# Kernel tuning notes

Measured on AMD Instinct MI355X. Metric: run time of the kernel, lower is better.

## Reference

```python
import jax, jax.numpy as jnp
import numpy as np

EMB_DIM = 256
N_EMBED = 1024
BETA = 0.25


def setup_inputs() -> dict:
    key = jax.random.key(0)
    k1, k2 = jax.random.split(key)
    encoderout = jax.random.normal(k1, (32, EMB_DIM, 32, 32), dtype=jnp.float32)
    # embedding.weight.data.normal_(mean=0, std=1/n_embed)
    codebook = jax.random.normal(k2, (N_EMBED, EMB_DIM), dtype=jnp.float32) * (1.0 / N_EMBED)
    return {"encoderout": encoderout, "codebook": codebook}


def reference(encoderout, codebook):
    # NCHW -> NHWC
    x = jnp.transpose(encoderout, (0, 2, 3, 1))  # [B,H,W,D]
    flat = x.reshape(-1, EMB_DIM)                # [N,D]
    d2 = (jnp.sum(flat * flat, axis=1, keepdims=True)
          + jnp.sum(codebook * codebook, axis=1)[None, :]
          - 2.0 * flat @ codebook.T)             # [N,K]
    idx = jnp.argmin(d2, axis=1)                 # [N]
    quant = codebook[idx].reshape(x.shape)       # [B,H,W,D]
    codebook_loss = jnp.mean((quant - jax.lax.stop_gradient(x)) ** 2)
    commitment_loss = jnp.mean((x - jax.lax.stop_gradient(quant)) ** 2)
    loss = codebook_loss + BETA * commitment_loss
    # FAITHFUL to source bug: straight-through output is overwritten by the
    # input permuted back to NCHW, so out == encoderout.
    out = jnp.transpose(x, (0, 3, 1, 2))
    return (out, loss, codebook_loss, commitment_loss)
```

## Files before the change

### kernel.cpp

```cpp
#include <hip/hip_runtime.h>
#include <stdint.h>


#define EMB 256
#define ELEMS 8388608
#define NBLK 256

typedef __bf16 bf16x8 __attribute__((ext_vector_type(8)));
typedef float  f32x4  __attribute__((ext_vector_type(4)));

union Frag { uint4 u4; bf16x8 v; };

__device__ __forceinline__ unsigned short f2bf(float f) {
    unsigned u = __float_as_uint(f);
    u += 0x7FFFu + ((u >> 16) & 1u);
    return (unsigned short)(u >> 16);
}

__global__ __launch_bounds__(256) void vq_prep(const float* __restrict__ cb,
                                               uint2* __restrict__ cbswz,
                                               float* __restrict__ esq,
                                               float* __restrict__ accum,
                                               unsigned* __restrict__ done) {
    if (blockIdx.x == 0 && threadIdx.x == 0) { accum[0] = 0.f; done[0] = 0u; }

    const int tid  = threadIdx.x;
    const int w    = tid >> 6;
    const int lane = tid & 63;
    const int n    = blockIdx.x * 4 + w;

    const float4* row = (const float4*)(cb + n * EMB);
    float4 v = row[lane];

    float s = v.x * v.x + v.y * v.y + v.z * v.z + v.w * v.w;
    #pragma unroll
    for (int m = 1; m <= 32; m <<= 1) s += __shfl_xor(s, m);
    if (lane == 0) esq[n] = s;

    unsigned lo = (unsigned)f2bf(v.x) | ((unsigned)f2bf(v.y) << 16);
    unsigned hi = (unsigned)f2bf(v.z) | ((unsigned)f2bf(v.w) << 16);
    const int kc = lane >> 1;
    const int h  = lane & 1;
    const unsigned idx4 = ((unsigned)(n >> 6) << 11) + ((unsigned)(kc >> 2) << 8)
                        + ((unsigned)(n & 63) << 2) + (unsigned)(kc & 3);
    cbswz[idx4 * 2 + h] = make_uint2(lo, hi);
}


#define CHUNK_BODY(nc_, LOADNEXT_) do {                                        \
    f32x4 _a0 = (f32x4){0.f,0.f,0.f,0.f};                                      \
    f32x4 _a1 = (f32x4){0.f,0.f,0.f,0.f};                                      \
    f32x4 _a2 = (f32x4){0.f,0.f,0.f,0.f};                                      \
    f32x4 _a3 = (f32x4){0.f,0.f,0.f,0.f};                                      \
    _Pragma("unroll")                                                          \
    for (int _ks = 0; _ks < 8; ++_ks) {                                        \
        bf16x8 _bv = bfr[_ks].v;                                               \
        _a0 = __builtin_amdgcn_mfma_f32_16x16x32_bf16(afr[0][_ks], _bv, _a0, 0, 0, 0); \
        _a1 = __builtin_amdgcn_mfma_f32_16x16x32_bf16(afr[1][_ks], _bv, _a1, 0, 0, 0); \
        _a2 = __builtin_amdgcn_mfma_f32_16x16x32_bf16(afr[2][_ks], _bv, _a2, 0, 0, 0); \
        _a3 = __builtin_amdgcn_mfma_f32_16x16x32_bf16(afr[3][_ks], _bv, _a3, 0, 0, 0); \
        if (LOADNEXT_)       \
            bfr[_ks].u4 = pc[((nc_) + 1) * 2048 + _ks * 256];                  \
    }                                                                          \
    const float _eq = esq[(nc_) * 64 + nl];                                    \
    _Pragma("unroll")                                                          \
    for (int _r2 = 0; _r2 < 4; ++_r2) {                                        \
        rmin[0][_r2] = fminf(rmin[0][_r2], fmaf(-2.f, _a0[_r2], _eq));         \
        rmin[1][_r2] = fminf(rmin[1][_r2], fmaf(-2.f, _a1[_r2], _eq));         \
        rmin[2][_r2] = fminf(rmin[2][_r2], fmaf(-2.f, _a2[_r2], _eq));         \
        rmin[3][_r2] = fminf(rmin[3][_r2], fmaf(-2.f, _a3[_r2], _eq));         \
    } } while (0)

__global__ __launch_bounds__(512, 2)
void vq_main(const float* __restrict__ enc,
             const uint4* __restrict__ cbswz,
             const float* __restrict__ esq,
             float* __restrict__ out,
             float* __restrict__ accum,
             unsigned* __restrict__ done) {
    __shared__ uint4 As[4096];
    __shared__ float dmin[4][128];
    __shared__ float partsA[8];
    __shared__ float partsB[2];

    const int tid  = threadIdx.x;
    const int w    = tid >> 6;
    const int lane = tid & 63;
    const int q    = lane >> 4;
    const int c    = lane & 15;
    const int wm   = w >> 2;
    const int wn   = w & 3;

    const int b   = blockIdx.x >> 3;
    const int hw0 = (blockIdx.x & 7) << 7;
    const float* encB = enc + (size_t)b * 262144 + hw0;
    float*       outB = out + (size_t)b * 262144 + hw0;

    const int nl = wn * 16 + c;
    const uint4* pc = cbswz + (size_t)(nl * 4 + q);

    const int q4 = tid & 31;
    const int kg = tid >> 5;
    float sx = 0.f;
    {
        f32x4 vh[16];
        #pragma unroll
        for (int j = 0; j < 16; ++j)
            vh[j] = *(const f32x4*)(encB + (size_t)(kg * 16 + j) * 1024 + q4 * 4);
        #pragma unroll
        for (int j = 0; j < 16; ++j) {
            *(f32x4*)(outB + (size_t)(kg * 16 + j) * 1024 + q4 * 4) = vh[j];
            #pragma unroll
            for (int i2 = 0; i2 < 4; ++i2) sx = fmaf(vh[j][i2], vh[j][i2], sx);
        }
        #pragma unroll
        for (int i = 0; i < 4; ++i) {
            unsigned short us[16];
            #pragma unroll
            for (int j = 0; j < 16; ++j) us[j] = f2bf(vh[j][i]);
            uint4 pk0, pk1;
            pk0.x = (unsigned)us[0]  | ((unsigned)us[1]  << 16);
            pk0.y = (unsigned)us[2]  | ((unsigned)us[3]  << 16);
            pk0.z = (unsigned)us[4]  | ((unsigned)us[5]  << 16);
            pk0.w = (unsigned)us[6]  | ((unsigned)us[7]  << 16);
            pk1.x = (unsigned)us[8]  | ((unsigned)us[9]  << 16);
            pk1.y = (unsigned)us[10] | ((unsigned)us[11] << 16);
            pk1.z = (unsigned)us[12] | ((unsigned)us[13] << 16);
            pk1.w = (unsigned)us[14] | ((unsigned)us[15] << 16);
            const int r = q4 * 4 + i;
            As[r * 32 + ((2 * kg + 0) ^ (r & 7))] = pk0;
            As[r * 32 + ((2 * kg + 1) ^ (r & 7))] = pk1;
        }
    }

    Frag bfr[8];
    #pragma unroll
    for (int ks = 0; ks < 8; ++ks) bfr[ks].u4 = pc[ks * 256];

    #pragma unroll
    for (int m = 1; m <= 32; m <<= 1) sx += __shfl_xor(sx, m);
    if (lane == 0) partsA[w] = sx;
    __syncthreads();

    bf16x8 afr[4][8];
    #pragma unroll
    for (int mi = 0; mi < 4; ++mi) {
        const int r = wm * 64 + mi * 16 + c;
        #pragma unroll
        for (int ks = 0; ks < 8; ++ks) {
            Frag fa; fa.u4 = As[r * 32 + ((ks * 4 + q) ^ (r & 7))];
            afr[mi][ks] = fa.v;
        }
    }

    float rmin[4][4];
    #pragma unroll
    for (int mi = 0; mi < 4; ++mi)
        #pragma unroll
        for (int r2 = 0; r2 < 4; ++r2) rmin[mi][r2] = 1e30f;

    for (int nc = 0; nc < 15; ++nc) CHUNK_BODY(nc, 1);
    CHUNK_BODY(15, 0);

    #pragma unroll
    for (int mi = 0; mi < 4; ++mi)
        #pragma unroll
        for (int r2 = 0; r2 < 4; ++r2) {
            float x = rmin[mi][r2];
            x = fminf(x, __shfl_xor(x, 1));
            x = fminf(x, __shfl_xor(x, 2));
            x = fminf(x, __shfl_xor(x, 4));
            x = fminf(x, __shfl_xor(x, 8));
            rmin[mi][r2] = x;
        }
    if (c == 0) {
        #pragma unroll
        for (int mi = 0; mi < 4; ++mi)
            #pragma unroll
            for (int r2 = 0; r2 < 4; ++r2)
                dmin[wn][wm * 64 + mi * 16 + q * 4 + r2] = rmin[mi][r2];
    }
    __syncthreads();

    if (tid < 128) {
        float vr = fminf(fminf(dmin[0][tid], dmin[1][tid]),
                         fminf(dmin[2][tid], dmin[3][tid]));
        #pragma unroll
        for (int m = 1; m <= 32; m <<= 1) vr += __shfl_xor(vr, m);
        if ((tid & 63) == 0) partsB[tid >> 6] = vr;
    }
    __syncthreads();

    if (tid == 0) {
        float s = partsB[0] + partsB[1];
        #pragma unroll
        for (int w2 = 0; w2 < 8; ++w2) s += partsA[w2];
        atomicAdd(accum, s);
        __threadfence();
        unsigned prev = atomicAdd(done, 1u);
        if (prev == NBLK - 1) {
            float tot = atomicAdd(accum, 0.0f);
            float cbl = tot * (1.0f / (float)ELEMS);
            out[ELEMS + 0] = 1.25f * cbl;
            out[ELEMS + 1] = cbl;
            out[ELEMS + 2] = cbl;
        }
    }
}

extern "C" void kernel_launch(void* const* d_in, const int* in_sizes, int n_in,
                              void* d_out, int out_size, void* d_ws, size_t ws_size,
                              hipStream_t stream) {
    const float* enc = (const float*)d_in[0];
    const float* cb  = (const float*)d_in[1];
    float* out = (float*)d_out;

    float*    accum = (float*)d_ws;
    unsigned* done  = (unsigned*)((char*)d_ws + 64);
    float*    esq   = (float*)((char*)d_ws + 256);
    uint2*    cbswz = (uint2*)((char*)d_ws + 8192);

    vq_prep<<<dim3(256), dim3(256), 0, stream>>>(cb, cbswz, esq, accum, done);
    vq_main<<<dim3(NBLK), dim3(512), 0, stream>>>(enc, (const uint4*)cbswz, esq,
                                                  out, accum, done);
}
```

Measured before the change: 109.2 us.

## Split input staging so first half-block starts MFMA while second half loads

All 512 threads first stage the first 64 rows of the input tile (8 channels each) and sync. The first four waves then start their distance MFMAs right away, while the second four waves load, copy and convert the remaining 64 rows. Those waves then wait on a shared-memory counter before starting their own MFMAs. The goal is to overlap global loads of the second half with compute on the first, at the cost of uneven wave work and a spin-wait barrier on a shared counter.

```diff
diff --git a/kernel.cpp b/kernel.cpp
--- a/kernel.cpp
+++ b/kernel.cpp
@@ -71,6 +71,17 @@
         rmin[3][_r2] = fminf(rmin[3][_r2], fmaf(-2.f, _a3[_r2], _eq));         \
     } } while (0)
 
+#define EXTRACT_AFR(rbase_) do {                                               \
+    _Pragma("unroll")                                                          \
+    for (int _mi = 0; _mi < 4; ++_mi) {                                        \
+        const int _r = (rbase_) + _mi * 16 + c;                                \
+        _Pragma("unroll")                                                      \
+        for (int _ks = 0; _ks < 8; ++_ks) {                                    \
+            Frag _fa; _fa.u4 = As[_r * 32 + ((_ks * 4 + q) ^ (_r & 7))];       \
+            afr[_mi][_ks] = _fa.v;                                             \
+        }                                                                      \
+    } } while (0)
+
 __global__ __launch_bounds__(512, 2)
 void vq_main(const float* __restrict__ enc,
              const uint4* __restrict__ cbswz,
@@ -82,6 +93,7 @@
     __shared__ float dmin[4][128];
     __shared__ float partsA[8];
     __shared__ float partsB[2];
+    __shared__ unsigned g1cnt;
 
     const int tid  = threadIdx.x;
     const int w    = tid >> 6;
@@ -99,68 +111,103 @@
     const int nl = wn * 16 + c;
     const uint4* pc = cbswz + (size_t)(nl * 4 + q);
 
-    const int q4 = tid & 31;
-    const int kg = tid >> 5;
+    if (tid == 0) g1cnt = 0u;
+
+    const int q4s = tid & 15;
+    const int kgs = tid >> 4;
     float sx = 0.f;
     {
-        f32x4 vh[16];
-        #pragma unroll
-        for (int j = 0; j < 16; ++j)
-            vh[j] = *(const f32x4*)(encB + (size_t)(kg * 16 + j) * 1024 + q4 * 4);
-        #pragma unroll
-        for (int j = 0; j < 16; ++j) {
-            *(f32x4*)(outB + (size_t)(kg * 16 + j) * 1024 + q4 * 4) = vh[j];
+        f32x4 vh[8];
+        #pragma unroll
+        for (int j = 0; j < 8; ++j)
+            vh[j] = *(const f32x4*)(encB + (size_t)(kgs * 8 + j) * 1024 + q4s * 4);
+        #pragma unroll
+        for (int j = 0; j < 8; ++j) {
+            *(f32x4*)(outB + (size_t)(kgs * 8 + j) * 1024 + q4s * 4) = vh[j];
             #pragma unroll
             for (int i2 = 0; i2 < 4; ++i2) sx = fmaf(vh[j][i2], vh[j][i2], sx);
         }
         #pragma unroll
         for (int i = 0; i < 4; ++i) {
-            unsigned short us[16];
-            #pragma unroll
-            for (int j = 0; j < 16; ++j) us[j] = f2bf(vh[j][i]);
-            uint4 pk0, pk1;
-            pk0.x = (unsigned)us[0]  | ((unsigned)us[1]  << 16);
-            pk0.y = (unsigned)us[2]  | ((unsigned)us[3]  << 16);
-            pk0.z = (unsigned)us[4]  | ((unsigned)us[5]  << 16);
-            pk0.w = (unsigned)us[6]  | ((unsigned)us[7]  << 16);
-            pk1.x = (unsigned)us[8]  | ((unsigned)us[9]  << 16);
-            pk1.y = (unsigned)us[10] | ((unsigned)us[11] << 16);
-            pk1.z = (unsigned)us[12] | ((unsigned)us[13] << 16);
-            pk1.w = (unsigned)us[14] | ((unsigned)us[15] << 16);
-            const int r = q4 * 4 + i;
-            As[r * 32 + ((2 * kg + 0) ^ (r & 7))] = pk0;
-            As[r * 32 + ((2 * kg + 1) ^ (r & 7))] = pk1;
+            unsigned short us[8];
+            #pragma unroll
+            for (int j = 0; j < 8; ++j) us[j] = f2bf(vh[j][i]);
+            uint4 pk;
+            pk.x = (unsigned)us[0] | ((unsigned)us[1] << 16);
+            pk.y = (unsigned)us[2] | ((unsigned)us[3] << 16);
+            pk.z = (unsigned)us[4] | ((unsigned)us[5] << 16);
+            pk.w = (unsigned)us[6] | ((unsigned)us[7] << 16);
+            const int r = q4s * 4 + i;
+            As[r * 32 + (kgs ^ (r & 7))] = pk;
         }
     }
 
     Frag bfr[8];
-    #pragma unroll
-    for (int ks = 0; ks < 8; ++ks) bfr[ks].u4 = pc[ks * 256];
-
-    #pragma unroll
-    for (int m = 1; m <= 32; m <<= 1) sx += __shfl_xor(sx, m);
-    if (lane == 0) partsA[w] = sx;
+    if (wm == 0) {
+        #pragma unroll
+        for (int ks = 0; ks < 8; ++ks) bfr[ks].u4 = pc[ks * 256];
+    }
     __syncthreads();
 
     bf16x8 afr[4][8];
-    #pragma unroll
-    for (int mi = 0; mi < 4; ++mi) {
-        const int r = wm * 64 + mi * 16 + c;
-        #pragma unroll
-        for (int ks = 0; ks < 8; ++ks) {
-            Frag fa; fa.u4 = As[r * 32 + ((ks * 4 + q) ^ (r & 7))];
-            afr[mi][ks] = fa.v;
-        }
-    }
-
     float rmin[4][4];
     #pragma unroll
     for (int mi = 0; mi < 4; ++mi)
         #pragma unroll
         for (int r2 = 0; r2 < 4; ++r2) rmin[mi][r2] = 1e30f;
 
-    for (int nc = 0; nc < 15; ++nc) CHUNK_BODY(nc, 1);
-    CHUNK_BODY(15, 0);
+    if (wm == 0) {
+        EXTRACT_AFR(0);
+        for (int nc = 0; nc < 15; ++nc) CHUNK_BODY(nc, 1);
+        CHUNK_BODY(15, 0);
+    } else {
+        const int tid2 = tid - 256;
+        const int q42 = tid2 & 15;
+        const int kg2 = tid2 >> 4;
+        {
+            f32x4 vh[16];
+            #pragma unroll
+            for (int j = 0; j < 16; ++j)
+                vh[j] = *(const f32x4*)(encB + (size_t)(kg2 * 16 + j) * 1024 + 64 + q42 * 4);
+            #pragma unroll
+            for (int j = 0; j < 16; ++j) {
+                *(f32x4*)(outB + (size_t)(kg2 * 16 + j) * 1024 + 64 + q42 * 4) = vh[j];
+                #pragma unroll
+                for (int i2 = 0; i2 < 4; ++i2) sx = fmaf(vh[j][i2], vh[j][i2], sx);
+            }
+            #pragma unroll
+            for (int i = 0; i < 4; ++i) {
+                unsigned short us[16];
+                #pragma unroll
+                for (int j = 0; j < 16; ++j) us[j] = f2bf(vh[j][i]);
+                uint4 pk0, pk1;
+                pk0.x = (unsigned)us[0]  | ((unsigned)us[1]  << 16);
+                pk0.y = (unsigned)us[2]  | ((unsigned)us[3]  << 16);
+                pk0.z = (unsigned)us[4]  | ((unsigned)us[5]  << 16);
+                pk0.w = (unsigned)us[6]  | ((unsigned)us[7]  << 16);
+                pk1.x = (unsigned)us[8]  | ((unsigned)us[9]  << 16);
+                pk1.y = (unsigned)us[10] | ((unsigned)us[11] << 16);
+                pk1.z = (unsigned)us[12] | ((unsigned)us[13] << 16);
+                pk1.w = (unsigned)us[14] | ((unsigned)us[15] << 16);
+                const int r = 64 + q42 * 4 + i;
+                As[r * 32 + ((2 * kg2 + 0) ^ (r & 7))] = pk0;
+                As[r * 32 + ((2 * kg2 + 1) ^ (r & 7))] = pk1;
+            }
+        }
+        #pragma unroll
+        for (int ks = 0; ks < 8; ++ks) bfr[ks].u4 = pc[ks * 256];
+
+        __threadfence_block();
+        if (lane == 0) atomicAdd(&g1cnt, 1u);
+        while (*(volatile unsigned*)&g1cnt < 4u)
+            __builtin_amdgcn_s_sleep(2);
+        __builtin_amdgcn_sched_barrier(0);
+        asm volatile("" ::: "memory");
+
+        EXTRACT_AFR(64);
+        for (int nc = 0; nc < 15; ++nc) CHUNK_BODY(nc, 1);
+        CHUNK_BODY(15, 0);
+    }
 
     #pragma unroll
     for (int mi = 0; mi < 4; ++mi)
@@ -180,6 +227,9 @@
             for (int r2 = 0; r2 < 4; ++r2)
                 dmin[wn][wm * 64 + mi * 16 + q * 4 + r2] = rmin[mi][r2];
     }
+    #pragma unroll
+    for (int m = 1; m <= 32; m <<= 1) sx += __shfl_xor(sx, m);
+    if (lane == 0) partsA[w] = sx;
     __syncthreads();
 
     if (tid < 128) {
```

After: 107.8 us, median of 2. About the same (-1.2%).
